# Optimization experiments

Measured on AMD Instinct MI355X. Metric: run time of the kernel, lower is better.

The kernel has to match this reference:

```python
import jax, jax.numpy as jnp
import numpy as np

N_VOX = 500000
P, S, K = 2048, 64, 8          # pixels(rays), samples per ray, voxel neighbors per sample
F_M, F_H = 64, 128             # voxel feature dim, mlp hidden dim
FREQ_PE = 4
DEPTH_MIN, DEPTH_MAX = 1.0, 80.0
RAY_SAMPLE_STEPS = 64.0
EPS = 1e-10
IN_FEAT = F_M + 3 * FREQ_PE * 2  # 88


def lrelu(x):
    return jnp.where(x >= 0, x, 0.1 * x)  # LeakyReLU(0.1)


def posenc(x, L=FREQ_PE):
    # NeRF positional encoding: sin/cos(2^i * x), i in [0, L)
    freqs = 2.0 ** jnp.arange(L, dtype=x.dtype)          # [L]
    ang = x[..., None] * freqs                            # [..., 3, L]
    enc = jnp.concatenate([jnp.sin(ang), jnp.cos(ang)], axis=-1)  # [..., 3, 2L]
    return enc.reshape(x.shape[:-1] + (x.shape[-1] * 2 * L,))


def setup_inputs() -> dict:
    key = jax.random.key(0)
    ks = jax.random.split(key, 16)

    def xavier(k, fan_in, fan_out):
        return jax.random.normal(k, (fan_in, fan_out), jnp.float32) / np.sqrt(fan_in)

    inp = {
        'map_xyz': jax.random.normal(ks[0], (N_VOX, 3), jnp.float32),
        'map_feat': jax.random.normal(ks[1], (N_VOX, F_M), jnp.float32) * 0.05,
        'ind_voxel': jax.random.randint(ks[2], (P, S, K), 0, N_VOX),
        'sample_xyz': jax.random.normal(ks[3], (P, S, 3), jnp.float32),
        'dist_to_cam': jax.random.uniform(ks[4], (P, S), jnp.float32) * RAY_SAMPLE_STEPS,
        'W0': xavier(ks[5], IN_FEAT, F_H), 'b0': jnp.full((F_H,), 0.01, jnp.float32),
        'W1': xavier(ks[6], F_H, F_H),     'b1': jnp.full((F_H,), 0.01, jnp.float32),
        'W2': xavier(ks[7], F_H, F_H),     'b2': jnp.full((F_H,), 0.01, jnp.float32),
        'Wa0': xavier(ks[8], F_H, F_H // 2), 'ba0': jnp.full((F_H // 2,), 0.01, jnp.float32),
        'Wa1': xavier(ks[9], F_H // 2, 1),   'ba1': jnp.full((1,), 0.01, jnp.float32),
        'Wr0': xavier(ks[10], F_H, F_H // 2), 'br0': jnp.full((F_H // 2,), 0.01, jnp.float32),
        'Wr1': xavier(ks[11], F_H // 2, 3),   'br1': jnp.full((3,), 0.01, jnp.float32),
    }
    return inp


def reference(map_xyz, map_feat, ind_voxel, sample_xyz, dist_to_cam,
              W0, b0, W1, b1, W2, b2, Wa0, ba0, Wa1, ba1, Wr0, br0, Wr1, br1):
    # ---- voxel -> sample messages (func_msg_voxel_to_sample) ----
    voxel_xyz = map_xyz[ind_voxel]                       # [P,S,K,3] gather
    feat = map_feat[ind_voxel]                           # [P,S,K,F_M] gather
    offset = sample_xyz[:, :, None, :] - voxel_xyz       # [P,S,K,3]
    h = jnp.concatenate([feat, posenc(offset)], axis=-1) # [P,S,K,88]
    h = lrelu(h @ W0 + b0)
    h = lrelu(h @ W1 + b1)
    h = lrelu(h @ W2 + b2)                               # [P,S,K,F_H]
    w = jnp.exp(-10.0 * jnp.linalg.norm(offset, axis=-1))  # [P,S,K]
    w = w / jnp.sum(w, axis=-1, keepdims=True)
    # ---- reduce over K neighbors (func_reduce_voxel_to_sample) ----
    feat_s = jnp.sum(h * w[..., None], axis=2)           # [P,S,F_H]
    a = lrelu(feat_s @ Wa0 + ba0)
    alpha = jax.nn.sigmoid(a @ Wa1 + ba1)                # [P,S,1]
    r = lrelu(feat_s @ Wr0 + br0)
    rgb = jax.nn.sigmoid(r @ Wr1 + br1)                  # [P,S,3]
    # ---- sample -> pixel volume rendering (func_reduce_sample_to_pixel) ----
    dist = DEPTH_MIN + DEPTH_MAX * dist_to_cam / RAY_SAMPLE_STEPS  # [P,S]
    ones = jnp.ones((P, 1, 1), alpha.dtype)
    trans = jnp.cumprod(jnp.concatenate([ones, 1.0 - alpha + EPS], axis=1), axis=1)[:, :-1, :]
    blend = alpha * trans                                # [P,S,1]
    pixel_rgb = jnp.sum(rgb * blend, axis=1)             # [P,3]
    pixel_d = jnp.sum(dist[..., None] * blend, axis=1)   # [P,1]
    acc = jnp.sum(blend, axis=1)                         # [P,1]
    return jnp.concatenate([pixel_rgb, pixel_d, acc], axis=-1)  # [P,5]
```

## Files before the change

### kernel.cpp

```cpp
#include <hip/hip_runtime.h>

typedef __bf16 bf16_t;
typedef __bf16 bf16x2 __attribute__((ext_vector_type(2)));
typedef __bf16 bf16x4 __attribute__((ext_vector_type(4)));
typedef __bf16 bf16x8 __attribute__((ext_vector_type(8)));
typedef float  f32x4  __attribute__((ext_vector_type(4)));
typedef int    i32x4  __attribute__((ext_vector_type(4)));

#define NPIX 2048
#define NS   64
#define NK   8
#define NSAMP (NPIX*NS)
#define NROWS (NSAMP*NK)
#define TROWS 64
#define NTILES (NROWS/TROWS)
#define GRID   512
#define NIT    16
#define XSTR 104
#define HSTR 136
#define QSTR 144

#define PK_W0 0
#define PK_W1 1536
#define PK_W2 3584
#define PK_WA 5632
#define PK_WR 6656
#define PK_TOT 7680

#define PKQ_OFF   122880
#define WS_AR_BYTES (122880 + 32768)

#define SW_Q 300.0f
#define S1_Q 62.0f
#define S2_Q 87.0f
#define DQ1S2 (S2_Q / (S1_Q * SW_Q))
#define DQ2   (1.0f / (S2_Q * SW_Q))
#define RMAGIC 12582912.f

__global__ void pack_weights(const float* __restrict__ W0, const float* __restrict__ W1,
                             const float* __restrict__ W2, const float* __restrict__ Wa0,
                             const float* __restrict__ Wr0, bf16_t* __restrict__ dst0) {
  int tid = blockIdx.x * blockDim.x + threadIdx.x;
  if (tid >= PK_TOT * 8) return;
  const float* src; bf16_t* dst; int e, KD, ND, KS; float scl = 1.f;
  if (tid < 12288)      { src = W0;  dst = dst0;         e = tid;         KD = 88;  ND = 128; KS = 3; scl = S1_Q; }
  else if (tid < 28672) { src = W1;  dst = dst0 + 12288; e = tid - 12288; KD = 128; ND = 128; KS = 4; }
  else if (tid < 45056) { src = W2;  dst = dst0 + 28672; e = tid - 28672; KD = 128; ND = 128; KS = 4; }
  else if (tid < 53248) { src = Wa0; dst = dst0 + 45056; e = tid - 45056; KD = 128; ND = 64;  KS = 4; }
  else                  { src = Wr0; dst = dst0 + 53248; e = tid - 53248; KD = 128; ND = 64;  KS = 4; }
  int j = e & 7, l = (e >> 3) & 63, f = e >> 9;
  int s = f % KS, t = f / KS;
  int row = s * 32 + (l >> 4) * 8 + j;
  int col = t * 16 + (l & 15);
  float v = (row < KD) ? src[row * ND + col] * scl : 0.f;
  dst[e] = (bf16_t)v;
}

__global__ void pack_w12_i8(const float* __restrict__ W1, const float* __restrict__ W2,
                            char* __restrict__ dstq) {
  int tid = blockIdx.x * blockDim.x + threadIdx.x;
  if (tid >= 2 * 16384) return;
  const float* src = (tid < 16384) ? W1 : W2;
  int e = tid & 16383;
  int j = e & 15, l = (e >> 4) & 63, f = e >> 10;
  int s = f & 1, t = f >> 1;
  int k = s * 64 + ((l >> 4) << 4) + j;
  int c = t * 16 + (l & 15);
  int iv = (int)rintf(src[k * 128 + c] * SW_Q);
  iv = iv > 127 ? 127 : (iv < -127 ? -127 : iv);
  dstq[tid] = (char)iv;
}

__device__ __forceinline__ float lrelu(float v) { return fmaxf(v, 0.1f * v); }
__device__ __forceinline__ float sigmoidf(float x) { return 1.f / (1.f + __expf(-x)); }

__device__ __forceinline__ float q8pre(float v) {
  float h = fmaxf(v, 0.1f * v);
  h = fminf(fmaxf(h, -127.f), 127.f);
  return h + RMAGIC;
}
__device__ __forceinline__ unsigned pack4(float r0, float r1, float r2, float r3) {
  unsigned t0 = __builtin_amdgcn_perm(__builtin_bit_cast(unsigned, r1),
                                      __builtin_bit_cast(unsigned, r0), 0x00000400u);
  unsigned t1 = __builtin_amdgcn_perm(__builtin_bit_cast(unsigned, r3),
                                      __builtin_bit_cast(unsigned, r2), 0x00000400u);
  return __builtin_amdgcn_perm(t1, t0, 0x05040100u);
}

__global__ __launch_bounds__(512, 4)
void nerf_main(const float* __restrict__ map_xyz, const float* __restrict__ map_feat,
               const int* __restrict__ ind, const float* __restrict__ sample_xyz,
               const float* __restrict__ b0g, const float* __restrict__ b1g,
               const float* __restrict__ b2g, const float* __restrict__ ba0g,
               const float* __restrict__ wa1g, const float* __restrict__ ba1g,
               const float* __restrict__ br0g, const float* __restrict__ wr1g,
               const float* __restrict__ br1g, const bf16_t* __restrict__ wpack,
               float* __restrict__ ar_out)
{
  __shared__ __align__(16) bf16_t sX[TROWS * XSTR];
  __shared__ __align__(16) char   sQ1[TROWS * QSTR];
  __shared__ __align__(16) char   sQ2[TROWS * QSTR];
  __shared__ __align__(16) bf16_t sH3[TROWS * HSTR];
  __shared__ __align__(16) bf16_t sFS[16 * HSTR];
  __shared__ __align__(16) bf16_t sAR[16 * HSTR];
  __shared__ __align__(16) bf16_t sFB[2048];
  __shared__ __align__(16) float sWtA[TROWS], sWtB[TROWS];
  __shared__ float sWsA[8], sWsB[8];
  __shared__ __align__(16) float sB0[128], sB1[128], sB2[128], sBH[128], sFBv[4];

  const int tid = threadIdx.x;
  const int wid = tid >> 6, l = tid & 63;
  const int q = l >> 4, n = l & 15;
  const int sr = tid >> 3, sp = tid & 7;

  const bf16x8* pk = (const bf16x8*)wpack;
  bf16x8 w0f[3], hdf[4];
#pragma unroll
  for (int s = 0; s < 3; s++) w0f[s] = pk[PK_W0 + (wid * 3 + s) * 64 + l];
#pragma unroll
  for (int s = 0; s < 4; s++)
    hdf[s] = pk[(wid < 4 ? PK_WA : PK_WR) + ((wid & 3) * 4 + s) * 64 + l];
  const i32x4* pq = (const i32x4*)((const char*)wpack + PKQ_OFF);
  i32x4 w1q[2], w2q[2];
#pragma unroll
  for (int s = 0; s < 2; s++) {
    w1q[s] = pq[(wid * 2 + s) * 64 + l];
    w2q[s] = pq[1024 + (wid * 2 + s) * 64 + l];
  }

  auto COMMIT = [&](int tile, bf16_t* X, float* wtbuf) {
    const int m = tile * TROWS + sr;
    const int idx = ind[m];
    const float4* fp = (const float4*)(map_feat + (size_t)idx * 64 + sp * 8);
    float4 f0 = fp[0], f1 = fp[1];
    bf16x8 v;
    v[0] = (bf16_t)f0.x; v[1] = (bf16_t)f0.y; v[2] = (bf16_t)f0.z; v[3] = (bf16_t)f0.w;
    v[4] = (bf16_t)f1.x; v[5] = (bf16_t)f1.y; v[6] = (bf16_t)f1.z; v[7] = (bf16_t)f1.w;
    *(bf16x8*)(X + sr * XSTR + sp * 8) = v;
    const int g = m >> 3;
    if (sp < 6) {
      const int d = sp >> 1;
      float o = sample_xyz[g * 3 + d] - map_xyz[idx * 3 + d];
      float s1 = __sinf(o), c1 = __cosf(o);
      float s2 = 2.f * s1 * c1, c2 = 1.f - 2.f * s1 * s1;
      float s4 = 2.f * s2 * c2, c4 = 1.f - 2.f * s2 * s2;
      float s8 = 2.f * s4 * c4, c8 = 1.f - 2.f * s4 * s4;
      bf16x4 e;
      if (sp & 1) { e[0] = (bf16_t)c1; e[1] = (bf16_t)c2; e[2] = (bf16_t)c4; e[3] = (bf16_t)c8; }
      else        { e[0] = (bf16_t)s1; e[1] = (bf16_t)s2; e[2] = (bf16_t)s4; e[3] = (bf16_t)s8; }
      *(bf16x4*)(X + sr * XSTR + 64 + d * 8 + (sp & 1) * 4) = e;
    } else if (sp == 6) {
      bf16x8 z = {};
      *(bf16x8*)(X + sr * XSTR + 88) = z;
    } else {
      float ox = sample_xyz[g * 3 + 0] - map_xyz[idx * 3 + 0];
      float oy = sample_xyz[g * 3 + 1] - map_xyz[idx * 3 + 1];
      float oz = sample_xyz[g * 3 + 2] - map_xyz[idx * 3 + 2];
      wtbuf[sr] = __expf(-10.f * sqrtf(ox * ox + oy * oy + oz * oz));
    }
  };

  auto L0 = [&](const bf16_t* X, char* Qout) {
    f32x4 bi = *(const f32x4*)(sB0 + wid * 16 + q * 4);
    f32x4 acc[4] = {bi, bi, bi, bi};
    const bf16_t* rb = X + n * XSTR + q * 8;
    char* wb = Qout + n * QSTR + wid * 16 + q * 4;
    __builtin_amdgcn_s_setprio(1);
#pragma unroll
    for (int st = 0; st < 4; st++)
#pragma unroll
      for (int s = 0; s < 3; s++) {
        bf16x8 b = *(const bf16x8*)(rb + st * 16 * XSTR + s * 32);
        acc[st] = __builtin_amdgcn_mfma_f32_16x16x32_bf16(w0f[s], b, acc[st], 0, 0, 0);
      }
    __builtin_amdgcn_s_setprio(0);
#pragma unroll
    for (int st = 0; st < 4; st++) {
      float r0 = q8pre(acc[st][0]), r1 = q8pre(acc[st][1]);
      float r2 = q8pre(acc[st][2]), r3 = q8pre(acc[st][3]);
      *(unsigned*)(wb + st * 16 * QSTR) = pack4(r0, r1, r2, r3);
    }
  };

  auto L1Q = [&](const char* Qin, char* Qout) {
    i32x4 acc[4] = {};
    const char* rb = Qin + n * QSTR + q * 16;
    char* wb = Qout + n * QSTR + wid * 16 + q * 4;
    f32x4 b1v = *(const f32x4*)(sB1 + wid * 16 + q * 4);
    __builtin_amdgcn_s_setprio(1);
#pragma unroll
    for (int st = 0; st < 4; st++)
#pragma unroll
      for (int s = 0; s < 2; s++) {
        i32x4 b = *(const i32x4*)(rb + st * 16 * QSTR + s * 64);
        acc[st] = __builtin_amdgcn_mfma_i32_16x16x64_i8(w1q[s], b, acc[st], 0, 0, 0);
      }
    __builtin_amdgcn_s_setprio(0);
#pragma unroll
    for (int st = 0; st < 4; st++) {
      float r[4];
#pragma unroll
      for (int i = 0; i < 4; i++)
        r[i] = q8pre(fmaf((float)acc[st][i], DQ1S2, b1v[i]));
      *(unsigned*)(wb + st * 16 * QSTR) = pack4(r[0], r[1], r[2], r[3]);
    }
  };

  auto L2Q = [&](const char* Qin, bf16_t* Hout) {
    i32x4 acc[4] = {};
    const char* rb = Qin + n * QSTR + q * 16;
    bf16_t* wb = Hout + n * HSTR + wid * 16 + q * 4;
    f32x4 b2v = *(const f32x4*)(sB2 + wid * 16 + q * 4);
    __builtin_amdgcn_s_setprio(1);
#pragma unroll
    for (int st = 0; st < 4; st++)
#pragma unroll
      for (int s = 0; s < 2; s++) {
        i32x4 b = *(const i32x4*)(rb + st * 16 * QSTR + s * 64);
        acc[st] = __builtin_amdgcn_mfma_i32_16x16x64_i8(w2q[s], b, acc[st], 0, 0, 0);
      }
    __builtin_amdgcn_s_setprio(0);
#pragma unroll
    for (int st = 0; st < 4; st++) {
      bf16x4 o;
#pragma unroll
      for (int i = 0; i < 4; i++) {
        float v = fmaf((float)acc[st][i], DQ2, b2v[i]);
        o[i] = (bf16_t)lrelu(v);
      }
      *(bf16x4*)(wb + st * 16 * HSTR) = o;
    }
  };

  auto KRED = [&](const bf16_t* Hin, const float* wt, const float* ws_, bf16_t* FS) {
    int g = tid >> 6;
    int c = (tid & 63) * 2;
    const bf16_t* kb = Hin + g * 8 * HSTR + c;
    float a0 = 0.f, a1 = 0.f;
#pragma unroll
    for (int k = 0; k < 8; k++) {
      float wk = wt[g * 8 + k];
      unsigned u = *(const unsigned*)(kb + k * HSTR);
      a0 += wk * __uint_as_float(u << 16);
      a1 += wk * __uint_as_float(u & 0xffff0000u);
    }
    float inv = 1.f / ws_[g];
    bf16x2 fo;
    fo[0] = (bf16_t)(a0 * inv);
    fo[1] = (bf16_t)(a1 * inv);
    *(bf16x2*)(FS + g * HSTR + c) = fo;
  };

  auto HEADS = [&](const bf16_t* FS, bf16_t* AR) {
    f32x4 ha = *(const f32x4*)(sBH + wid * 16 + q * 4);
    const bf16_t* rb = FS + n * HSTR + q * 8;
    __builtin_amdgcn_s_setprio(1);
#pragma unroll
    for (int s = 0; s < 4; s++) {
      bf16x8 b = *(const bf16x8*)(rb + s * 32);
      ha = __builtin_amdgcn_mfma_f32_16x16x32_bf16(hdf[s], b, ha, 0, 0, 0);
    }
    __builtin_amdgcn_s_setprio(0);
    if (n < 8) {
      const int base = (wid < 4) ? 64 : 0;
      bf16x4 o;
      o[0] = (bf16_t)lrelu(ha[0]);
      o[1] = (bf16_t)lrelu(ha[1]);
      o[2] = (bf16_t)lrelu(ha[2]);
      o[3] = (bf16_t)lrelu(ha[3]);
      *(bf16x4*)(AR + n * HSTR + base + (wid & 3) * 16 + q * 4) = o;
    }
  };

  auto FINALS = [&](int tile) {
    if (wid == 0) {
      f32x4 c = *(const f32x4*)sFBv;
      const bf16_t* ab = sFB + l * 8;
      const bf16_t* rb = sAR + n * HSTR + q * 8;
#pragma unroll
      for (int s = 0; s < 4; s++) {
        bf16x8 a = *(const bf16x8*)(ab + s * 512);
        bf16x8 b = *(const bf16x8*)(rb + s * 32);
        c = __builtin_amdgcn_mfma_f32_16x16x32_bf16(a, b, c, 0, 0, 0);
      }
      if (q == 0 && n < 8) {
        float4 o;
        o.x = sigmoidf(c[0]);
        o.y = sigmoidf(c[1]);
        o.z = sigmoidf(c[2]);
        o.w = sigmoidf(c[3]);
        ((float4*)ar_out)[tile * 8 + n] = o;
      }
    }
  };

  for (int i = tid; i < 8 * HSTR; i += 512) {
    sFS[8 * HSTR + i] = (bf16_t)0.f;
    sAR[8 * HSTR + i] = (bf16_t)0.f;
  }
  {
    int e0 = tid * 4;
    int jb = e0 & 7, ll = (e0 >> 3) & 63, s = e0 >> 9;
    int m = ll & 15;
#pragma unroll
    for (int ii = 0; ii < 4; ii++) {
      int k = s * 32 + (ll >> 4) * 8 + jb + ii;
      float v = 0.f;
      if (k < 64)  { if (m < 3) v = wr1g[k * 3 + m]; }
      else         { if (m == 3) v = wa1g[k - 64]; }
      sFB[e0 + ii] = (bf16_t)v;
    }
  }
  if (tid < 128)      sB0[tid] = b0g[tid] * S1_Q;
  else if (tid < 256) sB1[tid - 128] = b1g[tid - 128] * S2_Q;
  else if (tid < 384) sB2[tid - 256] = b2g[tid - 256];
  else { int t = tid - 384; sBH[t] = (t < 64) ? ba0g[t] : br0g[t - 64]; }
  if (tid < 4) sFBv[tid] = (tid < 3) ? br1g[tid] : ba1g[0];
  __syncthreads();

  for (int it = 0; it <= NIT; ++it) {
    const bool a_on = (it < NIT);
    const bool b_on = (it > 0);
    const int tA  = (int)blockIdx.x + (2 * it) * GRID;
    const int tAp = (int)blockIdx.x + (2 * it - 2) * GRID;
    const int tB  = (int)blockIdx.x + (2 * it + 1) * GRID;
    const int tBp = (int)blockIdx.x + (2 * it - 1) * GRID;

    if (a_on) COMMIT(tA, sX, sWtA);
    if (b_on) L2Q(sQ2, sH3);
    if (b_on) FINALS(tAp);
    __syncthreads();

    if (a_on) L0(sX, sQ1);
    if (b_on) KRED(sH3, sWtB, sWsB, sFS);
    if (a_on && tid < 8) {
      float ss = 0.f;
#pragma unroll
      for (int k = 0; k < 8; k++) ss += sWtA[tid * 8 + k];
      sWsA[tid] = ss;
    }
    __syncthreads();

    if (a_on) L1Q(sQ1, sQ2);
    if (b_on) HEADS(sFS, sAR);
    __syncthreads();

    if (a_on) COMMIT(tB, sX, sWtB);
    if (a_on) L2Q(sQ2, sH3);
    if (b_on) FINALS(tBp);
    __syncthreads();

    if (it == NIT) break;

    L0(sX, sQ1);
    KRED(sH3, sWtA, sWsA, sFS);
    if (tid < 8) {
      float ss = 0.f;
#pragma unroll
      for (int k = 0; k < 8; k++) ss += sWtB[tid * 8 + k];
      sWsB[tid] = ss;
    }
    __syncthreads();

    L1Q(sQ1, sQ2);
    HEADS(sFS, sAR);
    __syncthreads();
  }
}

__global__ __launch_bounds__(512)
void render_kernel(const float* __restrict__ ar, const float* __restrict__ dcam,
                   float* __restrict__ out) {
  int ray = blockIdx.x * 8 + (threadIdx.x >> 6);
  int s = threadIdx.x & 63;
  float4 v = ((const float4*)ar)[ray * 64 + s];
  float alpha = v.w;
  float t = 1.f - alpha + 1e-10f;
  float p = t;
#pragma unroll
  for (int d = 1; d < 64; d <<= 1) {
    float o = __shfl_up(p, d);
    if (s >= d) p *= o;
  }
  float pm1 = __shfl_up(p, 1);
  float T = (s == 0) ? 1.f : pm1;
  float bl = alpha * T;
  float dist = 1.f + 1.25f * dcam[ray * 64 + s];
  float cr = v.x * bl, cg = v.y * bl, cb = v.z * bl, cd = dist * bl, ca = bl;
#pragma unroll
  for (int d = 32; d > 0; d >>= 1) {
    cr += __shfl_xor(cr, d);
    cg += __shfl_xor(cg, d);
    cb += __shfl_xor(cb, d);
    cd += __shfl_xor(cd, d);
    ca += __shfl_xor(ca, d);
  }
  if (s == 0) {
    out[ray * 5 + 0] = cr; out[ray * 5 + 1] = cg; out[ray * 5 + 2] = cb;
    out[ray * 5 + 3] = cd; out[ray * 5 + 4] = ca;
  }
}

extern "C" void kernel_launch(void* const* d_in, const int* in_sizes, int n_in,
                              void* d_out, int out_size, void* d_ws, size_t ws_size,
                              hipStream_t stream) {
  const float* map_xyz    = (const float*)d_in[0];
  const float* map_feat   = (const float*)d_in[1];
  const int*   ind        = (const int*)d_in[2];
  const float* sample_xyz = (const float*)d_in[3];
  const float* dist_cam   = (const float*)d_in[4];
  const float* W0  = (const float*)d_in[5];
  const float* b0  = (const float*)d_in[6];
  const float* W1  = (const float*)d_in[7];
  const float* b1  = (const float*)d_in[8];
  const float* W2  = (const float*)d_in[9];
  const float* b2  = (const float*)d_in[10];
  const float* Wa0 = (const float*)d_in[11];
  const float* ba0 = (const float*)d_in[12];
  const float* Wa1 = (const float*)d_in[13];
  const float* ba1 = (const float*)d_in[14];
  const float* Wr0 = (const float*)d_in[15];
  const float* br0 = (const float*)d_in[16];
  const float* Wr1 = (const float*)d_in[17];
  const float* br1 = (const float*)d_in[18];

  bf16_t* wpack = (bf16_t*)d_ws;
  char*   wq    = (char*)d_ws + PKQ_OFF;
  float*  ar    = (float*)((char*)d_ws + WS_AR_BYTES);

  pack_weights<<<240, 256, 0, stream>>>(W0, W1, W2, Wa0, Wr0, wpack);
  pack_w12_i8<<<128, 256, 0, stream>>>(W1, W2, wq);
  nerf_main<<<GRID, 512, 0, stream>>>(map_xyz, map_feat, ind, sample_xyz,
                                      b0, b1, b2, ba0, Wa1, ba1, br0, Wr1, br1,
                                      wpack, ar);
  render_kernel<<<256, 512, 0, stream>>>(ar, dist_cam, (float*)d_out);
}
```

Before: 359.4 us.

## Quantize layer-2 output to int8 and shrink LDS to fit six blocks per CU

Layer-2 output is now stored as int8 with an extra scale, replacing the bf16 buffer, and the neighbour reduction dequantizes it. The per-tile FS/AR buffers are halved, with guarded loads instead of zero-padded rows. Together these cut shared memory per block so occupancy can rise to 6 blocks per CU, and the grid grows to 768 blocks with per-tile bounds checks. This adds int8 rounding error on the last hidden layer and uneven work across blocks, since the last iteration is only partly filled.

```diff
diff --git a/kernel.cpp b/kernel.cpp
--- a/kernel.cpp
+++ b/kernel.cpp
@@ -14,8 +14,8 @@
 #define NROWS (NSAMP*NK)
 #define TROWS 64
 #define NTILES (NROWS/TROWS)
-#define GRID   512
-#define NIT    16
+#define GRID   768
+#define NITG   11
 #define XSTR 104
 #define HSTR 136
 #define QSTR 144
@@ -33,8 +33,9 @@
 #define SW_Q 300.0f
 #define S1_Q 62.0f
 #define S2_Q 87.0f
+#define S3_Q 76.0f
 #define DQ1S2 (S2_Q / (S1_Q * SW_Q))
-#define DQ2   (1.0f / (S2_Q * SW_Q))
+#define DQ2S3 (S3_Q / (S2_Q * SW_Q))
 #define RMAGIC 12582912.f
 
 __global__ void pack_weights(const float* __restrict__ W0, const float* __restrict__ W1,
@@ -87,7 +88,7 @@
   return __builtin_amdgcn_perm(t1, t0, 0x05040100u);
 }
 
-__global__ __launch_bounds__(512, 4)
+__global__ __launch_bounds__(512, 6)
 void nerf_main(const float* __restrict__ map_xyz, const float* __restrict__ map_feat,
                const int* __restrict__ ind, const float* __restrict__ sample_xyz,
                const float* __restrict__ b0g, const float* __restrict__ b1g,
@@ -100,9 +101,9 @@
   __shared__ __align__(16) bf16_t sX[TROWS * XSTR];
   __shared__ __align__(16) char   sQ1[TROWS * QSTR];
   __shared__ __align__(16) char   sQ2[TROWS * QSTR];
-  __shared__ __align__(16) bf16_t sH3[TROWS * HSTR];
-  __shared__ __align__(16) bf16_t sFS[16 * HSTR];
-  __shared__ __align__(16) bf16_t sAR[16 * HSTR];
+  __shared__ __align__(16) char   sQ3[TROWS * QSTR];
+  __shared__ __align__(16) bf16_t sFS[8 * HSTR];
+  __shared__ __align__(16) bf16_t sAR[8 * HSTR];
   __shared__ __align__(16) bf16_t sFB[2048];
   __shared__ __align__(16) float sWtA[TROWS], sWtB[TROWS];
   __shared__ float sWsA[8], sWsB[8];
@@ -206,10 +207,10 @@
     }
   };
 
-  auto L2Q = [&](const char* Qin, bf16_t* Hout) {
+  auto L2Q = [&](const char* Qin, char* Qout) {
     i32x4 acc[4] = {};
     const char* rb = Qin + n * QSTR + q * 16;
-    bf16_t* wb = Hout + n * HSTR + wid * 16 + q * 4;
+    char* wb = Qout + n * QSTR + wid * 16 + q * 4;
     f32x4 b2v = *(const f32x4*)(sB2 + wid * 16 + q * 4);
     __builtin_amdgcn_s_setprio(1);
 #pragma unroll
@@ -222,29 +223,27 @@
     __builtin_amdgcn_s_setprio(0);
 #pragma unroll
     for (int st = 0; st < 4; st++) {
-      bf16x4 o;
-#pragma unroll
-      for (int i = 0; i < 4; i++) {
-        float v = fmaf((float)acc[st][i], DQ2, b2v[i]);
-        o[i] = (bf16_t)lrelu(v);
-      }
-      *(bf16x4*)(wb + st * 16 * HSTR) = o;
-    }
-  };
-
-  auto KRED = [&](const bf16_t* Hin, const float* wt, const float* ws_, bf16_t* FS) {
+      float r[4];
+#pragma unroll
+      for (int i = 0; i < 4; i++)
+        r[i] = q8pre(fmaf((float)acc[st][i], DQ2S3, b2v[i]));
+      *(unsigned*)(wb + st * 16 * QSTR) = pack4(r[0], r[1], r[2], r[3]);
+    }
+  };
+
+  auto KRED = [&](const char* Qin, const float* wt, const float* ws_, bf16_t* FS) {
     int g = tid >> 6;
     int c = (tid & 63) * 2;
-    const bf16_t* kb = Hin + g * 8 * HSTR + c;
+    const char* kb = Qin + g * 8 * QSTR + c;
     float a0 = 0.f, a1 = 0.f;
 #pragma unroll
     for (int k = 0; k < 8; k++) {
       float wk = wt[g * 8 + k];
-      unsigned u = *(const unsigned*)(kb + k * HSTR);
-      a0 += wk * __uint_as_float(u << 16);
-      a1 += wk * __uint_as_float(u & 0xffff0000u);
-    }
-    float inv = 1.f / ws_[g];
+      int us = *(const unsigned short*)(kb + k * QSTR);
+      a0 = fmaf(wk, (float)((us << 24) >> 24), a0);
+      a1 = fmaf(wk, (float)((us << 16) >> 24), a1);
+    }
+    float inv = 1.f / (ws_[g] * S3_Q);
     bf16x2 fo;
     fo[0] = (bf16_t)(a0 * inv);
     fo[1] = (bf16_t)(a1 * inv);
@@ -254,12 +253,15 @@
   auto HEADS = [&](const bf16_t* FS, bf16_t* AR) {
     f32x4 ha = *(const f32x4*)(sBH + wid * 16 + q * 4);
     const bf16_t* rb = FS + n * HSTR + q * 8;
+    bf16x8 bb[4] = {};
+    if (n < 8) {
+#pragma unroll
+      for (int s = 0; s < 4; s++) bb[s] = *(const bf16x8*)(rb + s * 32);
+    }
     __builtin_amdgcn_s_setprio(1);
 #pragma unroll
-    for (int s = 0; s < 4; s++) {
-      bf16x8 b = *(const bf16x8*)(rb + s * 32);
-      ha = __builtin_amdgcn_mfma_f32_16x16x32_bf16(hdf[s], b, ha, 0, 0, 0);
-    }
+    for (int s = 0; s < 4; s++)
+      ha = __builtin_amdgcn_mfma_f32_16x16x32_bf16(hdf[s], bb[s], ha, 0, 0, 0);
     __builtin_amdgcn_s_setprio(0);
     if (n < 8) {
       const int base = (wid < 4) ? 64 : 0;
@@ -277,11 +279,15 @@
       f32x4 c = *(const f32x4*)sFBv;
       const bf16_t* ab = sFB + l * 8;
       const bf16_t* rb = sAR + n * HSTR + q * 8;
+      bf16x8 bb[4] = {};
+      if (n < 8) {
+#pragma unroll
+        for (int s = 0; s < 4; s++) bb[s] = *(const bf16x8*)(rb + s * 32);
+      }
 #pragma unroll
       for (int s = 0; s < 4; s++) {
         bf16x8 a = *(const bf16x8*)(ab + s * 512);
-        bf16x8 b = *(const bf16x8*)(rb + s * 32);
-        c = __builtin_amdgcn_mfma_f32_16x16x32_bf16(a, b, c, 0, 0, 0);
+        c = __builtin_amdgcn_mfma_f32_16x16x32_bf16(a, bb[s], c, 0, 0, 0);
       }
       if (q == 0 && n < 8) {
         float4 o;
@@ -294,10 +300,6 @@
     }
   };
 
-  for (int i = tid; i < 8 * HSTR; i += 512) {
-    sFS[8 * HSTR + i] = (bf16_t)0.f;
-    sAR[8 * HSTR + i] = (bf16_t)0.f;
-  }
   {
     int e0 = tid * 4;
     int jb = e0 & 7, ll = (e0 >> 3) & 63, s = e0 >> 9;
@@ -313,27 +315,29 @@
   }
   if (tid < 128)      sB0[tid] = b0g[tid] * S1_Q;
   else if (tid < 256) sB1[tid - 128] = b1g[tid - 128] * S2_Q;
-  else if (tid < 384) sB2[tid - 256] = b2g[tid - 256];
+  else if (tid < 384) sB2[tid - 256] = b2g[tid - 256] * S3_Q;
   else { int t = tid - 384; sBH[t] = (t < 64) ? ba0g[t] : br0g[t - 64]; }
   if (tid < 4) sFBv[tid] = (tid < 3) ? br1g[tid] : ba1g[0];
   __syncthreads();
 
-  for (int it = 0; it <= NIT; ++it) {
-    const bool a_on = (it < NIT);
-    const bool b_on = (it > 0);
+  for (int it = 0; it <= NITG; ++it) {
     const int tA  = (int)blockIdx.x + (2 * it) * GRID;
-    const int tAp = (int)blockIdx.x + (2 * it - 2) * GRID;
     const int tB  = (int)blockIdx.x + (2 * it + 1) * GRID;
-    const int tBp = (int)blockIdx.x + (2 * it - 1) * GRID;
-
-    if (a_on) COMMIT(tA, sX, sWtA);
-    if (b_on) L2Q(sQ2, sH3);
-    if (b_on) FINALS(tAp);
-    __syncthreads();
-
-    if (a_on) L0(sX, sQ1);
-    if (b_on) KRED(sH3, sWtB, sWsB, sFS);
-    if (a_on && tid < 8) {
+    const int tAp = tA - 2 * GRID;
+    const int tBp = tB - 2 * GRID;
+    const bool aC = (tA < NTILES);
+    const bool bC = (tB < NTILES);
+    const bool aP = (it > 0) && (tAp < NTILES);
+    const bool bP = (it > 0) && (tBp < NTILES);
+
+    if (aC) COMMIT(tA, sX, sWtA);
+    if (bP) L2Q(sQ2, sQ3);
+    if (aP) FINALS(tAp);
+    __syncthreads();
+
+    if (aC) L0(sX, sQ1);
+    if (bP) KRED(sQ3, sWtB, sWsB, sFS);
+    if (aC && tid < 8) {
       float ss = 0.f;
 #pragma unroll
       for (int k = 0; k < 8; k++) ss += sWtA[tid * 8 + k];
@@ -341,20 +345,18 @@
     }
     __syncthreads();
 
-    if (a_on) L1Q(sQ1, sQ2);
-    if (b_on) HEADS(sFS, sAR);
-    __syncthreads();
-
-    if (a_on) COMMIT(tB, sX, sWtB);
-    if (a_on) L2Q(sQ2, sH3);
-    if (b_on) FINALS(tBp);
-    __syncthreads();
-
-    if (it == NIT) break;
-
-    L0(sX, sQ1);
-    KRED(sH3, sWtA, sWsA, sFS);
-    if (tid < 8) {
+    if (aC) L1Q(sQ1, sQ2);
+    if (bP) HEADS(sFS, sAR);
+    __syncthreads();
+
+    if (bC) COMMIT(tB, sX, sWtB);
+    if (aC) L2Q(sQ2, sQ3);
+    if (bP) FINALS(tBp);
+    __syncthreads();
+
+    if (bC) L0(sX, sQ1);
+    if (aC) KRED(sQ3, sWtA, sWsA, sFS);
+    if (bC && tid < 8) {
       float ss = 0.f;
 #pragma unroll
       for (int k = 0; k < 8; k++) ss += sWtB[tid * 8 + k];
@@ -362,8 +364,8 @@
     }
     __syncthreads();
 
-    L1Q(sQ1, sQ2);
-    HEADS(sFS, sAR);
+    if (aC) HEADS(sFS, sAR);
+    if (bC) L1Q(sQ1, sQ2);
     __syncthreads();
   }
 }
```

After: 430.5 us. +19.8%, slower.
